# Optimization experiments

Measured on AMD Instinct MI355X. Metric: run time of the kernel, lower is better.

Reference implementation:

```python
import jax, jax.numpy as jnp
import numpy as np

B, S, D = 4, 2048, 1024  # batch, seq_len, model dim (= qk_dim = output_dim)


def setup_inputs() -> dict:
    key = jax.random.key(0)
    kq, kk, kv, kwq, kwk, kwv = jax.random.split(key, 6)
    q = jax.random.normal(kq, (B, S, D), dtype=jnp.float32)
    k = jax.random.normal(kk, (B, S, D), dtype=jnp.float32)
    v = jax.random.normal(kv, (B, S, D), dtype=jnp.float32)
    # causal mask, broadcast over batch
    mask = jnp.broadcast_to(jnp.tril(jnp.ones((S, S), dtype=bool)), (B, S, S))
    W_q = jax.random.uniform(kwq, (D, D), dtype=jnp.float32)
    W_k = jax.random.uniform(kwk, (D, D), dtype=jnp.float32)
    W_v = jax.random.uniform(kwv, (D, D), dtype=jnp.float32)
    return {"q": q, "k": k, "v": v, "mask": mask, "W_q": W_q, "W_k": W_k, "W_v": W_v}


def reference(q, k, v, mask, W_q, W_k, W_v):
    q1 = q @ W_q  # (B, S, D)
    k1 = k @ W_k  # (B, S, D)
    v1 = v @ W_v  # (B, S, D)
    qk = jnp.einsum('bij,bkj->bik', q1, k1)  # (B, S, S)
    qk = qk * jax.lax.rsqrt(float(k1.shape[-1]))
    neg_inf = jnp.finfo(jnp.float32).min
    qk = jnp.where(mask, qk, neg_inf)
    s = jax.nn.softmax(qk, axis=-1)
    return jnp.einsum('bij,bjk->bik', s, v1)
```

## Files before the change

### kernel.cpp

```cpp
#include <hip/hip_runtime.h>
#include <hip/hip_bf16.h>
#include <float.h>


typedef __attribute__((ext_vector_type(8))) short bf16x8;
typedef __attribute__((ext_vector_type(4))) float f32x4;

#define MFMA16 __builtin_amdgcn_mfma_f32_16x16x32_bf16

union U8 { bf16x8 v; unsigned w[4]; };

__device__ __forceinline__ ushort f2bf(float x) {
  union { float f; unsigned u; } v; v.f = x;
  unsigned r = v.u + 0x7fffu + ((v.u >> 16) & 1u);
  return (ushort)(r >> 16);
}
__device__ __forceinline__ float bf2f(ushort h) {
  union { unsigned u; float f; } v; v.u = ((unsigned)h) << 16;
  return v.f;
}
__device__ __forceinline__ void splitf(float x, ushort& hi, ushort& lo) {
  hi = f2bf(x);
  lo = f2bf(x - bf2f(hi));
}

__device__ __forceinline__ bf16x8 cvt8(const float* lp) {
  U8 H;
#pragma unroll
  for (int p = 0; p < 4; ++p) {
    const unsigned u0 = __float_as_uint(lp[2 * p]);
    const unsigned u1 = __float_as_uint(lp[2 * p + 1]);
    const unsigned r0 = (u0 + 0x7fffu + ((u0 >> 16) & 1u)) >> 16;
    const unsigned r1 = (u1 + 0x7fffu + ((u1 >> 16) & 1u)) & 0xffff0000u;
    H.w[p] = r0 | r1;
  }
  return H.v;
}

#define GLOAD16(gp, lp)                                                        \
  __builtin_amdgcn_global_load_lds(                                            \
      (const __attribute__((address_space(1))) void*)(gp),                     \
      (__attribute__((address_space(3))) void*)(lp), 16, 0, 0)

#define BARRIER() asm volatile("s_barrier" ::: "memory")
#define VMCNT8() asm volatile("s_waitcnt vmcnt(8)" ::: "memory")
#define VMCNT6() asm volatile("s_waitcnt vmcnt(6)" ::: "memory")
#define VMCNT0() asm volatile("s_waitcnt vmcnt(0)" ::: "memory")

__device__ __forceinline__ void stage_bf16_32(const ushort* g, int pitch,
                                              ushort* lds, int w, int lane) {
#pragma unroll
  for (int i = 0; i < 2; ++i) {
    const int c = w * 2 + i;
    const int row = c * 16 + (lane >> 2);
    const int kp = (lane & 3) * 8;
    GLOAD16(g + (size_t)row * pitch + kp, lds + c * 512);
  }
}
__device__ __forceinline__ void stage_f32_32(const float* g, int pitch,
                                             float* lds, int w, int lane) {
#pragma unroll
  for (int i = 0; i < 4; ++i) {
    const int c = w * 4 + i;
    const int row = c * 8 + (lane >> 3);
    const int kp = (lane & 7) * 4;
    GLOAD16(g + (size_t)row * pitch + kp, lds + c * 256);
  }
}

__device__ __forceinline__ bf16x8 rd32(const ushort* s, int row, int kg) {
  const int cb = (kg * 16) ^ (((row >> 1) & 3) << 4);
  return *reinterpret_cast<const bf16x8*>(&s[row * 32 + (cb >> 1)]);
}

__global__ __launch_bounds__(256) void wt_split(
    const float* __restrict__ q, const float* __restrict__ k,
    const float* __restrict__ W0, const float* __restrict__ W1,
    const float* __restrict__ W2, ushort* __restrict__ Th0,
    ushort* __restrict__ Tl0, ushort* __restrict__ Th1,
    ushort* __restrict__ Tl1, ushort* __restrict__ Th2,
    ushort* __restrict__ qh, ushort* __restrict__ ql,
    ushort* __restrict__ kh, ushort* __restrict__ kl) {
  __shared__ float t[32][33];
  const int f = blockIdx.x;
  if (f < 3072) {
    const int z = f >> 10, r10 = f & 1023;
    const int bx = r10 & 31, by = r10 >> 5;
    const float* W = z == 0 ? W0 : (z == 1 ? W1 : W2);
    ushort* Th = z == 0 ? Th0 : (z == 1 ? Th1 : Th2);
    ushort* Tl = z == 0 ? Tl0 : (z == 1 ? Tl1 : nullptr);
    const int r = threadIdx.x >> 3, c4 = (threadIdx.x & 7) * 4;
    const float4 x = *reinterpret_cast<const float4*>(
        &W[(size_t)(bx * 32 + r) * 1024 + by * 32 + c4]);
    t[r][c4] = x.x; t[r][c4 + 1] = x.y; t[r][c4 + 2] = x.z; t[r][c4 + 3] = x.w;
    __syncthreads();
    ushort h[4], l[4];
#pragma unroll
    for (int j = 0; j < 4; ++j) splitf(t[c4 + j][r], h[j], l[j]);
    const size_t o = (size_t)(by * 32 + r) * 1024 + bx * 32 + c4;
    *reinterpret_cast<ushort4*>(&Th[o]) = ushort4{h[0], h[1], h[2], h[3]};
    if (Tl)
      *reinterpret_cast<ushort4*>(&Tl[o]) = ushort4{l[0], l[1], l[2], l[3]};
  } else {
    const int fl = f - 3072;
    const float* X = (fl >> 11) ? k : q;
    ushort* H = (fl >> 11) ? kh : qh;
    ushort* L = (fl >> 11) ? kl : ql;
    const int n4 = 2097152;
    for (int i = (fl & 2047) * 256 + threadIdx.x; i < n4; i += 2048 * 256) {
      const float4 x = reinterpret_cast<const float4*>(X)[i];
      ushort h0, l0, h1, l1, h2, l2, h3, l3;
      splitf(x.x, h0, l0); splitf(x.y, h1, l1);
      splitf(x.z, h2, l2); splitf(x.w, h3, l3);
      reinterpret_cast<ushort4*>(H)[i] = ushort4{h0, h1, h2, h3};
      reinterpret_cast<ushort4*>(L)[i] = ushort4{l0, l1, l2, l3};
    }
  }
}

__global__ __launch_bounds__(512, 2) void proj_qk8(
    const ushort* __restrict__ Ah0, const ushort* __restrict__ Al0,
    const ushort* __restrict__ Ah1, const ushort* __restrict__ Al1,
    const ushort* __restrict__ Bh0, const ushort* __restrict__ Bl0,
    const ushort* __restrict__ Bh1, const ushort* __restrict__ Bl1,
    ushort* __restrict__ Oh0, ushort* __restrict__ Ol0,
    ushort* __restrict__ Oh1, ushort* __restrict__ Ol1) {
  __shared__ ushort Ahs[2][8192], Als[2][8192];
  __shared__ ushort Bhs[2][8192], Bls[2][8192];
  const int bid = blockIdx.x;
  const int fid = (bid & 7) * 32 + (bid >> 3);
  const int z = fid >> 7, r = fid & 127;
  const int yt = r >> 2, xt = r & 3;
  const ushort* Ahp = (z ? Ah1 : Ah0) + (size_t)yt * 256 * 1024;
  const ushort* Alp = (z ? Al1 : Al0) + (size_t)yt * 256 * 1024;
  const ushort* Bhp = (z ? Bh1 : Bh0) + (size_t)xt * 256 * 1024;
  const ushort* Blp = (z ? Bl1 : Bl0) + (size_t)xt * 256 * 1024;
  ushort* Oh = z ? Oh1 : Oh0;
  ushort* Ol = z ? Ol1 : Ol0;
  const int t = threadIdx.x;
  const int lane = t & 63, w = t >> 6;
  const int wm = w >> 2, wn = w & 3;
  const int lr = lane & 15, kg = lane >> 4;
  f32x4 acc[8][4] = {};

  auto stage_slab = [&](const ushort* g, ushort* lds, int k0) {
#pragma unroll
    for (int i = 0; i < 2; ++i) {
      const int c = t + i * 512;
      const int row = c >> 2;
      const int lcb = ((c & 3) * 16) ^ (((row >> 1) & 3) << 4);
      GLOAD16(g + (size_t)row * 1024 + k0 + (lcb >> 1), lds + c * 8);
    }
  };
  auto stage_tile = [&](int kt) {
    const int k0 = kt * 32;
    const int slot = kt & 1;
    stage_slab(Ahp, Ahs[slot], k0);
    stage_slab(Alp, Als[slot], k0);
    stage_slab(Bhp, Bhs[slot], k0);
    stage_slab(Blp, Bls[slot], k0);
  };

  stage_tile(0);
  for (int kt = 0; kt < 32; ++kt) {
    const int slot = kt & 1;
    if (kt + 1 < 32) {
      stage_tile(kt + 1);
      VMCNT8();
    } else {
      VMCNT0();
    }
    BARRIER();
    bf16x8 bh[4], bl[4];
#pragma unroll
    for (int n = 0; n < 4; ++n) {
      const int col = wn * 64 + n * 16 + lr;
      bh[n] = rd32(Bhs[slot], col, kg);
      bl[n] = rd32(Bls[slot], col, kg);
    }
#pragma unroll
    for (int mq = 0; mq < 2; ++mq) {
      bf16x8 ah[4], al[4];
#pragma unroll
      for (int m = 0; m < 4; ++m) {
        const int row = wm * 128 + (mq * 4 + m) * 16 + lr;
        ah[m] = rd32(Ahs[slot], row, kg);
        al[m] = rd32(Als[slot], row, kg);
      }
      __builtin_amdgcn_s_setprio(1);
#pragma unroll
      for (int m = 0; m < 4; ++m)
#pragma unroll
        for (int n = 0; n < 4; ++n) {
          acc[mq * 4 + m][n] = MFMA16(ah[m], bh[n], acc[mq * 4 + m][n], 0, 0, 0);
          acc[mq * 4 + m][n] = MFMA16(ah[m], bl[n], acc[mq * 4 + m][n], 0, 0, 0);
          acc[mq * 4 + m][n] = MFMA16(al[m], bh[n], acc[mq * 4 + m][n], 0, 0, 0);
        }
      __builtin_amdgcn_s_setprio(0);
    }
    BARRIER();
  }

#pragma unroll
  for (int m = 0; m < 8; ++m)
#pragma unroll
    for (int n = 0; n < 4; ++n)
#pragma unroll
      for (int reg = 0; reg < 4; ++reg) {
        const int gm = yt * 256 + wm * 128 + m * 16 + kg * 4 + reg;
        const int gn = xt * 256 + wn * 64 + n * 16 + lr;
        ushort h, l;
        splitf(acc[m][n][reg], h, l);
        Oh[(size_t)gm * 1024 + gn] = h;
        Ol[(size_t)gm * 1024 + gn] = l;
      }
}

__global__ __launch_bounds__(256) void qk2(
    const ushort* __restrict__ q1h, const ushort* __restrict__ q1l,
    const ushort* __restrict__ k1h, const ushort* __restrict__ k1l,
    float* __restrict__ scoresA, float* __restrict__ scoresB) {
  __shared__ ushort Ahs[2][4096], Als[2][4096];
  __shared__ ushort Bhs[2][4096], Bls[2][4096];
  const int f = blockIdx.x;
  const int s = (f & 7) * 136 + (f >> 3);
  const int z = s / 544;
  const int rem = s % 544;
  const int b = rem / 136;
  int p = rem % 136, ti = 0, accp = 0;
  while (accp + ti + 1 <= p) { accp += ti + 1; ++ti; }
  const int tj = p - accp;
  const int t = threadIdx.x, lane = t & 63, w = t >> 6;
  const int wr = w >> 1, wc = w & 1;
  const int lr = lane & 15, kg = lane >> 4;
  const int kh0 = z * 512;
  const ushort* qh = q1h + ((size_t)b * 2048 + ti * 128) * 1024 + kh0;
  const ushort* ql = q1l + ((size_t)b * 2048 + ti * 128) * 1024 + kh0;
  const ushort* kh = k1h + ((size_t)b * 2048 + tj * 128) * 1024 + kh0;
  const ushort* kl = k1l + ((size_t)b * 2048 + tj * 128) * 1024 + kh0;
  f32x4 acc[4][4] = {};

  auto stage_slab = [&](const ushort* g, ushort* lds, int k0) {
#pragma unroll
    for (int i = 0; i < 2; ++i) {
      const int c = t + i * 256;
      const int row = c >> 2;
      const int lcb = ((c & 3) * 16) ^ (((row >> 1) & 3) << 4);
      GLOAD16(g + (size_t)row * 1024 + k0 + (lcb >> 1), lds + c * 8);
    }
  };
  auto stage_tile = [&](int kt) {
    const int k0 = kt * 32;
    const int slot = kt & 1;
    stage_slab(qh, Ahs[slot], k0);
    stage_slab(ql, Als[slot], k0);
    stage_slab(kh, Bhs[slot], k0);
    stage_slab(kl, Bls[slot], k0);
  };

  stage_tile(0);
  for (int kt = 0; kt < 16; ++kt) {
    const int slot = kt & 1;
    if (kt + 1 < 16) {
      stage_tile(kt + 1);
      VMCNT8();
    } else {
      VMCNT0();
    }
    BARRIER();
    bf16x8 ah[4], al[4], bh[4], bl[4];
#pragma unroll
    for (int m = 0; m < 4; ++m) {
      const int row = wr * 64 + m * 16 + lr;
      ah[m] = rd32(Ahs[slot], row, kg);
      al[m] = rd32(Als[slot], row, kg);
    }
#pragma unroll
    for (int n = 0; n < 4; ++n) {
      const int col = wc * 64 + n * 16 + lr;
      bh[n] = rd32(Bhs[slot], col, kg);
      bl[n] = rd32(Bls[slot], col, kg);
    }
    __builtin_amdgcn_s_setprio(1);
#pragma unroll
    for (int m = 0; m < 4; ++m)
#pragma unroll
      for (int n = 0; n < 4; ++n) {
        acc[m][n] = MFMA16(ah[m], bh[n], acc[m][n], 0, 0, 0);
        acc[m][n] = MFMA16(ah[m], bl[n], acc[m][n], 0, 0, 0);
        acc[m][n] = MFMA16(al[m], bh[n], acc[m][n], 0, 0, 0);
      }
    __builtin_amdgcn_s_setprio(0);
    BARRIER();
  }
  const float sc = 0.03125f;
  float* st = (z ? scoresB : scoresA) + ((size_t)b * 136 + p) * 16384;
#pragma unroll
  for (int m = 0; m < 4; ++m)
#pragma unroll
    for (int n = 0; n < 4; ++n)
#pragma unroll
      for (int reg = 0; reg < 4; ++reg) {
        const int il = wr * 64 + m * 16 + kg * 4 + reg;
        const int jl = wc * 64 + n * 16 + lr;
        st[il * 128 + jl] = acc[m][n][reg] * sc;
      }
}

__global__ __launch_bounds__(256) void sm_projv(
    float* __restrict__ scoresA, const float* __restrict__ scoresB,
    const ushort* __restrict__ Wvt, const float* __restrict__ V,
    ushort* __restrict__ v1t) {
  __shared__ __align__(16) char smem[24576];
  const int tid = threadIdx.x, lane = tid & 63, w = tid >> 6;
  const int fg = blockIdx.x;
  if (fg >= 512) {
    float* red = reinterpret_cast<float*>(smem);
    const int f2 = fg - 512;
    const int b = f2 >> 11, r = f2 & 2047;
    const int ti = r >> 7, rl = r & 127, ncol = (ti + 1) * 128;
    const int valid = r + 1;
    const size_t tbase = ((size_t)b * 136 + (ti * (ti + 1)) / 2) * 16384;
    float* srowA = scoresA + tbase;
    const float* srowB = scoresB + tbase;

    float vals[2][4];
    float mx = -FLT_MAX;
#pragma unroll
    for (int c = 0; c < 2; ++c) {
      const int j = tid * 4 + c * 1024;
      if (j < ncol) {
        const size_t o = (size_t)(j >> 7) * 16384 + rl * 128 + (j & 127);
        const float4 a = *reinterpret_cast<const float4*>(srowA + o);
        const float4 bb = *reinterpret_cast<const float4*>(srowB + o);
        vals[c][0] = (j + 0 < valid) ? a.x + bb.x : -FLT_MAX;
        vals[c][1] = (j + 1 < valid) ? a.y + bb.y : -FLT_MAX;
        vals[c][2] = (j + 2 < valid) ? a.z + bb.z : -FLT_MAX;
        vals[c][3] = (j + 3 < valid) ? a.w + bb.w : -FLT_MAX;
      } else {
        vals[c][0] = vals[c][1] = vals[c][2] = vals[c][3] = -FLT_MAX;
      }
      mx = fmaxf(mx, fmaxf(fmaxf(vals[c][0], vals[c][1]),
                           fmaxf(vals[c][2], vals[c][3])));
    }
#pragma unroll
    for (int o = 32; o; o >>= 1) mx = fmaxf(mx, __shfl_xor(mx, o));
    if (lane == 0) red[w] = mx;
    __syncthreads();
    mx = fmaxf(fmaxf(red[0], red[1]), fmaxf(red[2], red[3]));

    float ex[2][4];
    float sum = 0.f;
#pragma unroll
    for (int c = 0; c < 2; ++c)
#pragma unroll
      for (int e = 0; e < 4; ++e) {
        const int j = tid * 4 + c * 1024 + e;
        ex[c][e] = (j < valid) ? __expf(vals[c][e] - mx) : 0.f;
        sum += ex[c][e];
      }
#pragma unroll
    for (int o = 32; o; o >>= 1) sum += __shfl_xor(sum, o);
    if (lane == 0) red[4 + w] = sum;
    __syncthreads();
    sum = red[4] + red[5] + red[6] + red[7];
    const float inv = 1.f / sum;
#pragma unroll
    for (int c = 0; c < 2; ++c) {
      const int j = tid * 4 + c * 1024;
      if (j < ncol) {
        ushort* pt =
            reinterpret_cast<ushort*>(srowA + (size_t)(j >> 7) * 16384);
        ushort4 pw;
        pw.x = f2bf(ex[c][0] * inv); pw.y = f2bf(ex[c][1] * inv);
        pw.z = f2bf(ex[c][2] * inv); pw.w = f2bf(ex[c][3] * inv);
        *reinterpret_cast<ushort4*>(&pt[rl * 256 + (j & 127)]) = pw;
      }
    }
  } else {
    ushort* Ahs = reinterpret_cast<ushort*>(smem);
    float* Bs = reinterpret_cast<float*>(smem + 8192);
    const int f2 = fg;
    const int yb = (f2 >> 3) & 7;
    const int xb = (f2 & 7) + ((f2 >> 6) << 3);
    const int wr = w >> 1, wc = w & 1;
    const int lr = lane & 15, kg = lane >> 4;
    const int m0 = yb * 128;
    const int n0 = xb * 128;
    f32x4 acc[4][4] = {};

    for (int k0 = 0; k0 < 1024; k0 += 32) {
      stage_bf16_32(Wvt + (size_t)m0 * 1024 + k0, 1024, Ahs, w, lane);
      stage_f32_32(V + (size_t)n0 * 1024 + k0, 1024, Bs, w, lane);
      __syncthreads();
      bf16x8 ah[4], bh[4];
#pragma unroll
      for (int m = 0; m < 4; ++m)
        ah[m] = *reinterpret_cast<bf16x8*>(
            &Ahs[(wr * 64 + m * 16 + lr) * 32 + kg * 8]);
#pragma unroll
      for (int n = 0; n < 4; ++n)
        bh[n] = cvt8(&Bs[(wc * 64 + n * 16 + lr) * 32 + kg * 8]);
#pragma unroll
      for (int m = 0; m < 4; ++m)
#pragma unroll
        for (int n = 0; n < 4; ++n)
          acc[m][n] = MFMA16(ah[m], bh[n], acc[m][n], 0, 0, 0);
      __syncthreads();
    }
#pragma unroll
    for (int m = 0; m < 4; ++m)
#pragma unroll
      for (int n = 0; n < 4; ++n)
#pragma unroll
        for (int reg = 0; reg < 4; ++reg) {
          const int gm = m0 + wr * 64 + m * 16 + kg * 4 + reg;
          const int gn = n0 + wc * 64 + n * 16 + lr;
          const int b = gn >> 11, jj = gn & 2047;
          v1t[((size_t)b << 21) + (size_t)gm * 2048 + jj] = f2bf(acc[m][n][reg]);
        }
  }
}

__global__ __launch_bounds__(256) void pv2(const float* __restrict__ scores,
                                           const ushort* __restrict__ v1t,
                                           float* __restrict__ out) {
  __shared__ ushort Ps[2][8192], Vs[2][4096];
  const int fl = blockIdx.x;
  const int s = (fl & 7) * 128 + (fl >> 3);
  const int b = s >> 8, rem = s & 255;
  const int ti = 15 - (rem >> 4);
  const int n0 = (rem & 15) * 64;
  const int t = threadIdx.x, lane = t & 63, w = t >> 6;
  const int wr = w >> 1, wc = w & 1;
  const int lr = lane & 15, kg = lane >> 4;
  const int tri_ti = (ti * (ti + 1)) / 2;
  const ushort* vbase = v1t + ((size_t)b << 21) + (size_t)n0 * 2048;
  const int nt = 2 * (ti + 1);
  f32x4 acc[4][2] = {};

  auto stage_tile = [&](int kt) {
    const int slot = kt & 1;
    const int k0 = kt * 64;
    const ushort* pt = reinterpret_cast<const ushort*>(
        scores + ((size_t)b * 136 + tri_ti + (k0 >> 7)) * 16384);
    const int kpo = (k0 & 64);
#pragma unroll
    for (int i = 0; i < 4; ++i) {
      const int c = t + i * 256;
      const int row = c >> 3;
      const int lcb = ((c & 7) * 16) ^ ((row & 7) << 4);
      GLOAD16(pt + (size_t)row * 256 + kpo + (lcb >> 1), Ps[slot] + c * 8);
    }
#pragma unroll
    for (int i = 0; i < 2; ++i) {
      const int c = t + i * 256;
      const int row = c >> 3;
      const int lcb = ((c & 7) * 16) ^ ((row & 7) << 4);
      GLOAD16(vbase + (size_t)row * 2048 + k0 + (lcb >> 1), Vs[slot] + c * 8);
    }
  };

  stage_tile(0);
  for (int kt = 0; kt < nt; ++kt) {
    const int slot = kt & 1;
    if (kt + 1 < nt) {
      stage_tile(kt + 1);
      VMCNT6();
    } else {
      VMCNT0();
    }
    BARRIER();
    bf16x8 pa[4][2], vb[2][2];
#pragma unroll
    for (int m = 0; m < 4; ++m)
#pragma unroll
      for (int ks = 0; ks < 2; ++ks) {
        const int row = wr * 64 + m * 16 + lr;
        const int cb = (ks * 64 + kg * 16) ^ ((row & 7) << 4);
        pa[m][ks] =
            *reinterpret_cast<const bf16x8*>(&Ps[slot][row * 64 + (cb >> 1)]);
      }
#pragma unroll
    for (int n = 0; n < 2; ++n)
#pragma unroll
      for (int ks = 0; ks < 2; ++ks) {
        const int col = wc * 32 + n * 16 + lr;
        const int cb = (ks * 64 + kg * 16) ^ ((col & 7) << 4);
        vb[n][ks] =
            *reinterpret_cast<const bf16x8*>(&Vs[slot][col * 64 + (cb >> 1)]);
      }
    __builtin_amdgcn_s_setprio(1);
#pragma unroll
    for (int m = 0; m < 4; ++m)
#pragma unroll
      for (int n = 0; n < 2; ++n)
#pragma unroll
        for (int ks = 0; ks < 2; ++ks)
          acc[m][n] = MFMA16(pa[m][ks], vb[n][ks], acc[m][n], 0, 0, 0);
    __builtin_amdgcn_s_setprio(0);
    BARRIER();
  }
#pragma unroll
  for (int m = 0; m < 4; ++m)
#pragma unroll
    for (int n = 0; n < 2; ++n)
#pragma unroll
      for (int reg = 0; reg < 4; ++reg) {
        const int gm = ti * 128 + wr * 64 + m * 16 + kg * 4 + reg;
        const int gn = n0 + wc * 32 + n * 16 + lr;
        out[((size_t)b * 2048 + gm) * 1024 + gn] = acc[m][n][reg];
      }
}

extern "C" void kernel_launch(void* const* d_in, const int* in_sizes, int n_in,
                              void* d_out, int out_size, void* d_ws,
                              size_t ws_size, hipStream_t stream) {
  const float* q = (const float*)d_in[0];
  const float* k = (const float*)d_in[1];
  const float* v = (const float*)d_in[2];
  const float* Wq = (const float*)d_in[4];
  const float* Wk = (const float*)d_in[5];
  const float* Wv = (const float*)d_in[6];
  float* out = (float*)d_out;

  char* ws = (char*)d_ws;
  const size_t SCORES_T = 35651584;
  float* scoresA = (float*)ws;
  float* scoresB = (float*)(ws + SCORES_T);
  ushort* qsh = (ushort*)ws;
  ushort* qsl = qsh + 8388608;
  ushort* ksh = qsh + 2 * 8388608;
  ushort* ksl = qsh + 3 * 8388608;
  ushort* q1hi = (ushort*)(ws + 2 * SCORES_T);
  ushort* q1lo = q1hi + 8388608;
  ushort* k1hi = q1hi + 2 * 8388608;
  ushort* k1lo = q1hi + 3 * 8388608;
  ushort* v1t = (ushort*)(ws + 2 * SCORES_T);
  ushort* Wqth = (ushort*)(ws + 2 * SCORES_T + 67108864);
  ushort* Wqtl = Wqth + 1048576;
  ushort* Wkth = Wqth + 2097152;
  ushort* Wktl = Wqth + 3145728;
  ushort* Wvt  = Wqth + 4194304;
  const size_t need = 2 * SCORES_T + 67108864 + 10485760;
  if (ws_size < need) return;

  dim3 blk(256);
  wt_split<<<dim3(7168), blk, 0, stream>>>(q, k, Wq, Wk, Wv, Wqth, Wqtl, Wkth,
                                           Wktl, Wvt, qsh, qsl, ksh, ksl);
  proj_qk8<<<dim3(256), dim3(512), 0, stream>>>(qsh, qsl, ksh, ksl, Wqth,
                                                Wqtl, Wkth, Wktl, q1hi, q1lo,
                                                k1hi, k1lo);
  qk2<<<dim3(1088), blk, 0, stream>>>(q1hi, q1lo, k1hi, k1lo, scoresA,
                                      scoresB);
  sm_projv<<<dim3(8704), blk, 0, stream>>>(scoresA, scoresB, Wvt, v, v1t);
  pv2<<<dim3(1024), blk, 0, stream>>>(scoresA, v1t, out);
}
```

Measured before the change: 289.9 us.

## Remove split-K in QK score kernel and drop second partial-score buffer

The QK^T score kernel no longer splits the 1024-wide reduction into two halves written to separate buffers. Each block now covers the full K range over 32 iterations, and the softmax kernel reads a single score buffer instead of adding two partials. This removes one full scores write and read pass, at the cost of halving the grid to 544 blocks with twice the work each, which may leave compute units less occupied.

```diff
diff --git a/kernel.cpp b/kernel.cpp
--- a/kernel.cpp
+++ b/kernel.cpp
@@ -219,25 +219,22 @@
 __global__ __launch_bounds__(256) void qk2(
     const ushort* __restrict__ q1h, const ushort* __restrict__ q1l,
     const ushort* __restrict__ k1h, const ushort* __restrict__ k1l,
-    float* __restrict__ scoresA, float* __restrict__ scoresB) {
+    float* __restrict__ scoresA) {
   __shared__ ushort Ahs[2][4096], Als[2][4096];
   __shared__ ushort Bhs[2][4096], Bls[2][4096];
   const int f = blockIdx.x;
-  const int s = (f & 7) * 136 + (f >> 3);
-  const int z = s / 544;
-  const int rem = s % 544;
-  const int b = rem / 136;
-  int p = rem % 136, ti = 0, accp = 0;
+  const int s = (f & 7) * 68 + (f >> 3);
+  const int b = s / 136;
+  int p = s % 136, ti = 0, accp = 0;
   while (accp + ti + 1 <= p) { accp += ti + 1; ++ti; }
   const int tj = p - accp;
   const int t = threadIdx.x, lane = t & 63, w = t >> 6;
   const int wr = w >> 1, wc = w & 1;
   const int lr = lane & 15, kg = lane >> 4;
-  const int kh0 = z * 512;
-  const ushort* qh = q1h + ((size_t)b * 2048 + ti * 128) * 1024 + kh0;
-  const ushort* ql = q1l + ((size_t)b * 2048 + ti * 128) * 1024 + kh0;
-  const ushort* kh = k1h + ((size_t)b * 2048 + tj * 128) * 1024 + kh0;
-  const ushort* kl = k1l + ((size_t)b * 2048 + tj * 128) * 1024 + kh0;
+  const ushort* qh = q1h + ((size_t)b * 2048 + ti * 128) * 1024;
+  const ushort* ql = q1l + ((size_t)b * 2048 + ti * 128) * 1024;
+  const ushort* kh = k1h + ((size_t)b * 2048 + tj * 128) * 1024;
+  const ushort* kl = k1l + ((size_t)b * 2048 + tj * 128) * 1024;
   f32x4 acc[4][4] = {};
 
   auto stage_slab = [&](const ushort* g, ushort* lds, int k0) {
@@ -259,9 +256,9 @@
   };
 
   stage_tile(0);
-  for (int kt = 0; kt < 16; ++kt) {
+  for (int kt = 0; kt < 32; ++kt) {
     const int slot = kt & 1;
-    if (kt + 1 < 16) {
+    if (kt + 1 < 32) {
       stage_tile(kt + 1);
       VMCNT8();
     } else {
@@ -294,7 +291,7 @@
     BARRIER();
   }
   const float sc = 0.03125f;
-  float* st = (z ? scoresB : scoresA) + ((size_t)b * 136 + p) * 16384;
+  float* st = scoresA + ((size_t)b * 136 + p) * 16384;
 #pragma unroll
   for (int m = 0; m < 4; ++m)
 #pragma unroll
@@ -308,9 +305,8 @@
 }
 
 __global__ __launch_bounds__(256) void sm_projv(
-    float* __restrict__ scoresA, const float* __restrict__ scoresB,
-    const ushort* __restrict__ Wvt, const float* __restrict__ V,
-    ushort* __restrict__ v1t) {
+    float* __restrict__ scoresA, const ushort* __restrict__ Wvt,
+    const float* __restrict__ V, ushort* __restrict__ v1t) {
   __shared__ __align__(16) char smem[24576];
   const int tid = threadIdx.x, lane = tid & 63, w = tid >> 6;
   const int fg = blockIdx.x;
@@ -322,7 +318,6 @@
     const int valid = r + 1;
     const size_t tbase = ((size_t)b * 136 + (ti * (ti + 1)) / 2) * 16384;
     float* srowA = scoresA + tbase;
-    const float* srowB = scoresB + tbase;
 
     float vals[2][4];
     float mx = -FLT_MAX;
@@ -332,11 +327,10 @@
       if (j < ncol) {
         const size_t o = (size_t)(j >> 7) * 16384 + rl * 128 + (j & 127);
         const float4 a = *reinterpret_cast<const float4*>(srowA + o);
-        const float4 bb = *reinterpret_cast<const float4*>(srowB + o);
-        vals[c][0] = (j + 0 < valid) ? a.x + bb.x : -FLT_MAX;
-        vals[c][1] = (j + 1 < valid) ? a.y + bb.y : -FLT_MAX;
-        vals[c][2] = (j + 2 < valid) ? a.z + bb.z : -FLT_MAX;
-        vals[c][3] = (j + 3 < valid) ? a.w + bb.w : -FLT_MAX;
+        vals[c][0] = (j + 0 < valid) ? a.x : -FLT_MAX;
+        vals[c][1] = (j + 1 < valid) ? a.y : -FLT_MAX;
+        vals[c][2] = (j + 2 < valid) ? a.z : -FLT_MAX;
+        vals[c][3] = (j + 3 < valid) ? a.w : -FLT_MAX;
       } else {
         vals[c][0] = vals[c][1] = vals[c][2] = vals[c][3] = -FLT_MAX;
       }
@@ -527,7 +521,6 @@
   char* ws = (char*)d_ws;
   const size_t SCORES_T = 35651584;
   float* scoresA = (float*)ws;
-  float* scoresB = (float*)(ws + SCORES_T);
   ushort* qsh = (ushort*)ws;
   ushort* qsl = qsh + 8388608;
   ushort* ksh = qsh + 2 * 8388608;
@@ -551,8 +544,7 @@
   proj_qk8<<<dim3(256), dim3(512), 0, stream>>>(qsh, qsl, ksh, ksl, Wqth,
                                                 Wqtl, Wkth, Wktl, q1hi, q1lo,
                                                 k1hi, k1lo);
-  qk2<<<dim3(1088), blk, 0, stream>>>(q1hi, q1lo, k1hi, k1lo, scoresA,
-                                      scoresB);
-  sm_projv<<<dim3(8704), blk, 0, stream>>>(scoresA, scoresB, Wvt, v, v1t);
+  qk2<<<dim3(544), blk, 0, stream>>>(q1hi, q1lo, k1hi, k1lo, scoresA);
+  sm_projv<<<dim3(8704), blk, 0, stream>>>(scoresA, Wvt, v, v1t);
   pv2<<<dim3(1024), blk, 0, stream>>>(scoresA, v1t, out);
 }
```

Measured after the change: 301.8 us. +4.1%, slower.
